# Optimization experiments

Hardware: AMD Instinct MI355X
Metric: run time of the kernel (lower is better)

## Reference

```python
import jax, jax.numpy as jnp
import numpy as np


def gcn_conv(x, edge_index, W, b):
    """PyG GCNConv: linear transform, add self-loops, symmetric D^-1/2 A D^-1/2 aggregation, bias."""
    n = x.shape[0]
    h = x @ W  # [N, out] - transform before propagate (small out dim)
    loop = jnp.arange(n, dtype=edge_index.dtype)
    src = jnp.concatenate([edge_index[0], loop])
    dst = jnp.concatenate([edge_index[1], loop])
    deg = jax.ops.segment_sum(jnp.ones_like(dst, dtype=h.dtype), dst, num_segments=n)
    dinv = jnp.where(deg > 0, jax.lax.rsqrt(deg), 0.0)
    norm = dinv[src] * dinv[dst]  # [E+N]
    out = jax.ops.segment_sum(h[src] * norm[:, None], dst, num_segments=n)
    return out + b


def setup_inputs() -> dict:
    key = jax.random.key(0)
    k1, k2, k3, k4, k5, k6 = jax.random.split(key, 6)
    N, F_in, H, C, E = 100000, 128, 16, 2, 3200000
    x = jax.random.normal(k1, (N, F_in), dtype=jnp.float32)
    edge_index = jax.random.randint(k2, (2, E), 0, N, dtype=jnp.int32)
    # Glorot-style init for GCNConv weights
    W1 = jax.random.normal(k3, (F_in, H), dtype=jnp.float32) * (1.0 / np.sqrt(F_in))
    b1 = jnp.zeros((H,), dtype=jnp.float32)
    W2 = jax.random.normal(k4, (H, C), dtype=jnp.float32) * (1.0 / np.sqrt(H))
    b2 = jnp.zeros((C,), dtype=jnp.float32)
    return {"x": x, "edge_index": edge_index, "W1": W1, "b1": b1, "W2": W2, "b2": b2}


def reference(x, edge_index, W1, b1, W2, b2):
    h = gcn_conv(x, edge_index, W1, b1)
    h = jax.nn.relu(h)
    # F.dropout(training=self.training): eval mode -> identity (deterministic reference)
    h = gcn_conv(h, edge_index, W2, b2)
    return jax.nn.log_softmax(h, axis=1)
```

## Files before the change

kernel.cpp:

```cpp
#include <hip/hip_runtime.h>
#include <hip/hip_bf16.h>
#include <math.h>


#define F_IN 128
#define H1 16
#define C_OUT 2
#define SBS 1024
#define LOG_SBS 10
#define NSB_MAX 128
#define SRC_MASK 0x3FFFFF
#define CH1 4096
#define SLICE 128
#define NSLICE (SBS / SLICE)
#define PCAP 5632

typedef int ix4 __attribute__((ext_vector_type(4)));

__device__ __forceinline__ float bflo(unsigned u) { return __uint_as_float(u << 16); }
__device__ __forceinline__ float bfhi(unsigned u) { return __uint_as_float(u & 0xFFFF0000u); }

__global__ __launch_bounds__(256) void k_cnt(
    const int* __restrict__ dst0, int* __restrict__ cntm, int E, int NSB, int nblk) {
    __shared__ int sc[NSB_MAX];
    int t = threadIdx.x;
    if (t < NSB_MAX) sc[t] = 0;
    __syncthreads();
    int e0 = blockIdx.x * CH1, e1 = min(e0 + CH1, E);
    int n4 = (e1 - e0) >> 2;
    const ix4* d4 = (const ix4*)(dst0 + e0);
    for (int i = t; i < n4; i += 256) {
        ix4 d = __builtin_nontemporal_load(&d4[i]);
        atomicAdd(&sc[((unsigned)d.x) >> LOG_SBS], 1);
        atomicAdd(&sc[((unsigned)d.y) >> LOG_SBS], 1);
        atomicAdd(&sc[((unsigned)d.z) >> LOG_SBS], 1);
        atomicAdd(&sc[((unsigned)d.w) >> LOG_SBS], 1);
    }
    for (int e = e0 + n4 * 4 + t; e < e1; e += 256)
        atomicAdd(&sc[((unsigned)dst0[e]) >> LOG_SBS], 1);
    __syncthreads();
    for (int b = t; b < NSB; b += 256)
        cntm[(size_t)b * nblk + blockIdx.x] = sc[b];
}

__global__ __launch_bounds__(1024) void k_cscan(
    int* __restrict__ cntm, int* __restrict__ tot, int* __restrict__ rp,
    int NSB, int nblk, int E) {
    __shared__ int s[1024];
    int b = blockIdx.x, t = threadIdx.x;
    int* row = cntm + (size_t)b * nblk;
    int own = (t < nblk) ? row[t] : 0;
    s[t] = own;
    __syncthreads();
    for (int off = 1; off < 1024; off <<= 1) {
        int v = (t >= off) ? s[t - off] : 0;
        __syncthreads();
        s[t] += v;
        __syncthreads();
    }
    if (t < nblk) row[t] = s[t] - own;
    if (t == 0) tot[b] = s[1023];
    if (b == 0 && t == 0) rp[NSB * SBS] = E;
}

__global__ __launch_bounds__(256) void k_scat1(
    const int* __restrict__ src0, const int* __restrict__ dst0,
    const int* __restrict__ cntm, unsigned* __restrict__ packed1,
    int E, int NSB, int nblk, int CAP) {
    __shared__ int lcur[NSB_MAX];
    int t = threadIdx.x, blk = blockIdx.x;
    for (int b = t; b < NSB; b += 256)
        lcur[b] = b * CAP + cntm[(size_t)b * nblk + blk];
    __syncthreads();
    int e0 = blk * CH1, e1 = min(e0 + CH1, E);
    int n4 = (e1 - e0) >> 2;
    const ix4* d4 = (const ix4*)(dst0 + e0);
    const ix4* s4 = (const ix4*)(src0 + e0);
    for (int i = t; i < n4; i += 256) {
        ix4 d = __builtin_nontemporal_load(&d4[i]);
        ix4 s = __builtin_nontemporal_load(&s4[i]);
        {
            unsigned dd = (unsigned)d.x;
            int pos = atomicAdd(&lcur[dd >> LOG_SBS], 1);
            packed1[pos] = (unsigned)s.x | ((dd & (SBS - 1)) << 22);
        }
        {
            unsigned dd = (unsigned)d.y;
            int pos = atomicAdd(&lcur[dd >> LOG_SBS], 1);
            packed1[pos] = (unsigned)s.y | ((dd & (SBS - 1)) << 22);
        }
        {
            unsigned dd = (unsigned)d.z;
            int pos = atomicAdd(&lcur[dd >> LOG_SBS], 1);
            packed1[pos] = (unsigned)s.z | ((dd & (SBS - 1)) << 22);
        }
        {
            unsigned dd = (unsigned)d.w;
            int pos = atomicAdd(&lcur[dd >> LOG_SBS], 1);
            packed1[pos] = (unsigned)s.w | ((dd & (SBS - 1)) << 22);
        }
    }
    for (int e = e0 + n4 * 4 + t; e < e1; e += 256) {
        unsigned dd = (unsigned)dst0[e];
        int pos = atomicAdd(&lcur[dd >> LOG_SBS], 1);
        packed1[pos] = (unsigned)src0[e] | ((dd & (SBS - 1)) << 22);
    }
}

__global__ __launch_bounds__(1024) void k_hist(
    const unsigned* __restrict__ packed1, const int* __restrict__ tot,
    int* __restrict__ rp, float* __restrict__ dinv, int N, int NSB, int CAP) {
    __shared__ int cnt[SBS];
    __shared__ int s2[SBS];
    __shared__ int sbase[NSB_MAX];
    int b = blockIdx.x, t = threadIdx.x;
    if (t < NSB_MAX) sbase[t] = (t < NSB) ? tot[t] : 0;
    cnt[t] = 0;
    __syncthreads();
    if (t == 0) {
        int run = 0;
        #pragma unroll 4
        for (int i = 0; i < NSB_MAX; ++i) { int c = sbase[i]; sbase[i] = run; run += c; }
    }
    __syncthreads();
    int cntb = tot[b];
    int e0 = b * CAP, e1 = e0 + cntb;
    int obase = sbase[b];
    int n4 = cntb >> 2;
    const ix4* p4 = (const ix4*)(packed1 + e0);
    for (int i = t; i < n4; i += 1024) {
        ix4 p = p4[i];
        atomicAdd(&cnt[((unsigned)p.x) >> 22], 1);
        atomicAdd(&cnt[((unsigned)p.y) >> 22], 1);
        atomicAdd(&cnt[((unsigned)p.z) >> 22], 1);
        atomicAdd(&cnt[((unsigned)p.w) >> 22], 1);
    }
    for (int e = e0 + n4 * 4 + t; e < e1; e += 1024)
        atomicAdd(&cnt[packed1[e] >> 22], 1);
    __syncthreads();
    int c = cnt[t];
    s2[t] = c;
    __syncthreads();
    for (int off = 1; off < 1024; off <<= 1) {
        int v = (t >= off) ? s2[t - off] : 0;
        __syncthreads();
        s2[t] += v;
        __syncthreads();
    }
    int ep = s2[t] - c;
    int node = (b << LOG_SBS) + t;
    rp[node] = obase + ep;
    if (node < N) dinv[node] = rsqrtf((float)(c + 1));
}

__global__ __launch_bounds__(512) void k_place(
    const unsigned* __restrict__ packed1, const int* __restrict__ tot,
    const int* __restrict__ rp, int* __restrict__ packed2,
    int NSB, int PADB, int CAP) {
    __shared__ int cur[SLICE];
    __shared__ int lbuf[PCAP];
    int bid = blockIdx.x;
    int s = bid / PADB, b = bid - s * PADB;
    if (b >= NSB) return;
    int t = threadIdx.x;
    int node0 = (b << LOG_SBS) + s * SLICE;
    int g0 = rp[node0];
    if (t < SLICE) cur[t] = rp[node0 + t] - g0;
    int slice_len = rp[node0 + SLICE] - g0;
    __syncthreads();
    int cntb = tot[b];
    int e0 = b * CAP, e1 = e0 + cntb;
    int n4 = cntb >> 2;
    const ix4* p4 = (const ix4*)(packed1 + e0);
    for (int i = t; i < n4; i += 512) {
        ix4 p = p4[i];
        {
            unsigned nd = ((unsigned)p.x) >> 22;
            if ((nd >> 7) == (unsigned)s) {
                int pos = atomicAdd(&cur[nd & (SLICE - 1)], 1);
                if (pos < PCAP) lbuf[pos] = p.x & SRC_MASK;
            }
        }
        {
            unsigned nd = ((unsigned)p.y) >> 22;
            if ((nd >> 7) == (unsigned)s) {
                int pos = atomicAdd(&cur[nd & (SLICE - 1)], 1);
                if (pos < PCAP) lbuf[pos] = p.y & SRC_MASK;
            }
        }
        {
            unsigned nd = ((unsigned)p.z) >> 22;
            if ((nd >> 7) == (unsigned)s) {
                int pos = atomicAdd(&cur[nd & (SLICE - 1)], 1);
                if (pos < PCAP) lbuf[pos] = p.z & SRC_MASK;
            }
        }
        {
            unsigned nd = ((unsigned)p.w) >> 22;
            if ((nd >> 7) == (unsigned)s) {
                int pos = atomicAdd(&cur[nd & (SLICE - 1)], 1);
                if (pos < PCAP) lbuf[pos] = p.w & SRC_MASK;
            }
        }
    }
    for (int e = e0 + n4 * 4 + t; e < e1; e += 512) {
        unsigned p = packed1[e];
        unsigned nd = p >> 22;
        if ((nd >> 7) == (unsigned)s) {
            int pos = atomicAdd(&cur[nd & (SLICE - 1)], 1);
            if (pos < PCAP) lbuf[pos] = (int)(p & SRC_MASK);
        }
    }
    __syncthreads();
    int lim = min(slice_len, PCAP);
    for (int i = t; i < lim; i += 512)
        packed2[g0 + i] = lbuf[i];
}

__global__ __launch_bounds__(256) void k_gemm1(
    const float* __restrict__ x, const float* __restrict__ W1,
    const float* __restrict__ dinv, __hip_bfloat16* __restrict__ h1b, int N) {
    __shared__ float w[F_IN * H1];
    __shared__ float xt[16 * F_IN];
    int tid = threadIdx.x;
    int node0 = blockIdx.x * 16;

    const float4* W14 = (const float4*)W1;
    float4* w4 = (float4*)w;
    for (int i = tid; i < F_IN * H1 / 4; i += 256) w4[i] = W14[i];

    const float4* x4 = (const float4*)x;
    float4* xt4 = (float4*)xt;
    for (int i = tid; i < 16 * F_IN / 4; i += 256) {
        int r = i >> 5;
        int node = node0 + r;
        xt4[i] = (node < N) ? x4[(size_t)node * 32 + (i & 31)]
                            : make_float4(0.f, 0.f, 0.f, 0.f);
    }
    __syncthreads();

    int nsub = tid >> 4, f = tid & 15;
    int node = node0 + nsub;
    if (node < N) {
        const float* xr = xt + nsub * F_IN;
        float acc = 0.0f;
        #pragma unroll 16
        for (int k = 0; k < F_IN; ++k)
            acc = fmaf(xr[k], w[k * H1 + f], acc);
        h1b[(size_t)node * H1 + f] = __float2bfloat16(acc * dinv[node]);
    }
}

__global__ __launch_bounds__(256) void k_agg1(
    const int* __restrict__ packed2, const int* __restrict__ rp,
    const __hip_bfloat16* __restrict__ h1b, const float* __restrict__ dinv,
    const float* __restrict__ b1, const float* __restrict__ W2,
    float* __restrict__ h2s, int N) {
    int tid = blockIdx.x * 256 + threadIdx.x;
    int n = tid >> 2, q = tid & 3;
    if (n >= N) return;
    const uint2* hv = (const uint2*)h1b;
    float a[4];
    {
        uint2 s = hv[(size_t)n * 4 + q];
        a[0] = bflo(s.x); a[1] = bfhi(s.x); a[2] = bflo(s.y); a[3] = bfhi(s.y);
    }
    int e = rp[n], e1 = rp[n + 1];
    for (; e + 8 <= e1; e += 8) {
        int p[8];
        #pragma unroll
        for (int u = 0; u < 8; ++u) p[u] = packed2[e + u];
        uint2 v[8];
        #pragma unroll
        for (int u = 0; u < 8; ++u) v[u] = hv[(size_t)p[u] * 4 + q];
        #pragma unroll
        for (int u = 0; u < 8; ++u) {
            a[0] += bflo(v[u].x); a[1] += bfhi(v[u].x);
            a[2] += bflo(v[u].y); a[3] += bfhi(v[u].y);
        }
    }
    for (; e < e1; ++e) {
        uint2 v = hv[(size_t)packed2[e] * 4 + q];
        a[0] += bflo(v.x); a[1] += bfhi(v.x); a[2] += bflo(v.y); a[3] += bfhi(v.y);
    }
    float dv = dinv[n];
    float c0 = 0.f, c1 = 0.f;
    #pragma unroll
    for (int j = 0; j < 4; ++j) {
        int f = q * 4 + j;
        float vv = fmaxf(fmaf(a[j], dv, b1[f]), 0.f);
        c0 = fmaf(vv, W2[f * C_OUT + 0], c0);
        c1 = fmaf(vv, W2[f * C_OUT + 1], c1);
    }
    c0 += __shfl_xor(c0, 1);
    c1 += __shfl_xor(c1, 1);
    c0 += __shfl_xor(c0, 2);
    c1 += __shfl_xor(c1, 2);
    if (q == 0)
        ((float2*)h2s)[n] = make_float2(c0 * dv, c1 * dv);
}

__global__ __launch_bounds__(256) void k_agg2(
    const int* __restrict__ packed2, const int* __restrict__ rp,
    const float* __restrict__ h2s, const float* __restrict__ dinv,
    const float* __restrict__ b2, float* __restrict__ out, int N) {
    int tid = blockIdx.x * 256 + threadIdx.x;
    int n = tid >> 1, q = tid & 1;
    if (n >= N) return;
    float a = h2s[2 * (size_t)n + q];
    int e = rp[n], e1 = rp[n + 1];
    for (; e + 8 <= e1; e += 8) {
        int p[8];
        #pragma unroll
        for (int u = 0; u < 8; ++u) p[u] = packed2[e + u];
        float v[8];
        #pragma unroll
        for (int u = 0; u < 8; ++u) v[u] = h2s[2 * (size_t)p[u] + q];
        #pragma unroll
        for (int u = 0; u < 8; ++u) a += v[u];
    }
    for (; e < e1; ++e) a += h2s[2 * (size_t)packed2[e] + q];
    float dv = dinv[n];
    a = fmaf(a, dv, b2[q]);
    float other = __shfl_xor(a, 1);
    if (q == 0) {
        float a0 = a, a1 = other;
        float m = fmaxf(a0, a1);
        float lse = m + logf(expf(a0 - m) + expf(a1 - m));
        ((float2*)out)[n] = make_float2(a0 - lse, a1 - lse);
    }
}

extern "C" void kernel_launch(void* const* d_in, const int* in_sizes, int n_in,
                              void* d_out, int out_size, void* d_ws, size_t ws_size,
                              hipStream_t stream) {
    const float* x  = (const float*)d_in[0];
    const int* ei   = (const int*)d_in[1];
    const float* W1 = (const float*)d_in[2];
    const float* b1 = (const float*)d_in[3];
    const float* W2 = (const float*)d_in[4];
    const float* b2 = (const float*)d_in[5];
    float* out = (float*)d_out;

    const int N = in_sizes[0] / F_IN;
    const int E = in_sizes[1] / 2;
    const int* src0 = ei;
    const int* dst0 = ei + E;

    const int NSB = (N + SBS - 1) >> LOG_SBS;
    const int nblk = (E + CH1 - 1) / CH1;
    const int PADB = (NSB + 7) & ~7;
    int expSB = (int)(((long long)E << LOG_SBS) / N);
    int CAP = (expSB + expSB / 8 + 2048 + 15) & ~15;

    size_t off = 0;
    float* wsf = (float*)d_ws;
    auto take = [&](size_t nf) { float* p = wsf + off; off += (nf + 3) & ~(size_t)3; return p; };
    float* dinv    = take(N);
    __hip_bfloat16* h1b = (__hip_bfloat16*)take((size_t)N * H1 / 2);
    float* h2s     = take((size_t)N * C_OUT);
    unsigned* packed1 = (unsigned*)take((size_t)NSB * CAP);
    int*   packed2 = (int*)take(E);
    int*   cntm    = (int*)take((size_t)NSB * nblk);
    int*   tot     = (int*)take(NSB_MAX);
    int*   rp      = (int*)take((size_t)NSB * SBS + 1);

    k_cnt<<<nblk, 256, 0, stream>>>(dst0, cntm, E, NSB, nblk);
    k_cscan<<<NSB, 1024, 0, stream>>>(cntm, tot, rp, NSB, nblk, E);
    k_scat1<<<nblk, 256, 0, stream>>>(src0, dst0, cntm, packed1, E, NSB, nblk, CAP);
    k_hist<<<NSB, 1024, 0, stream>>>(packed1, tot, rp, dinv, N, NSB, CAP);
    k_place<<<NSLICE * PADB, 512, 0, stream>>>(packed1, tot, rp, packed2, NSB, PADB, CAP);
    k_gemm1<<<(N + 15) / 16, 256, 0, stream>>>(x, W1, dinv, h1b, N);
    k_agg1<<<(4 * N + 255) / 256, 256, 0, stream>>>(packed2, rp, h1b, dinv, b1, W2, h2s, N);
    k_agg2<<<(2 * N + 255) / 256, 256, 0, stream>>>(packed2, rp, h2s, dinv, b2, out, N);
}
```

Before: 141.0 us.

## Fuse gemm1 into count kernel and aggregation-1 into placement kernel

The dense x@W1 transform now runs as extra blocks of the edge-count kernel, so the two independent stages share one launch. The dinv row scaling of h1 moves into the histogram kernel, which rescales each bf16 row in place once the degree is known. The first aggregation is folded into the placement kernel: each slice gathers neighbours straight from its shared-memory source list instead of re-reading packed2 from global memory. This cuts two launches and one global pass over the edge list. In exchange, the placement kernel gets heavier and relies on slices fitting PCAP, and the extra bf16 rounding step changes numerics slightly.

```diff
diff --git a/kernel.cpp b/kernel.cpp
--- a/kernel.cpp
+++ b/kernel.cpp
@@ -20,27 +20,58 @@
 __device__ __forceinline__ float bflo(unsigned u) { return __uint_as_float(u << 16); }
 __device__ __forceinline__ float bfhi(unsigned u) { return __uint_as_float(u & 0xFFFF0000u); }
 
-__global__ __launch_bounds__(256) void k_cnt(
-    const int* __restrict__ dst0, int* __restrict__ cntm, int E, int NSB, int nblk) {
+__global__ __launch_bounds__(256) void k_cnt_gemm1(
+    const int* __restrict__ dst0, int* __restrict__ cntm,
+    const float* __restrict__ x, const float* __restrict__ W1,
+    __hip_bfloat16* __restrict__ h1b,
+    int E, int NSB, int nblk, int N) {
     __shared__ int sc[NSB_MAX];
+    __shared__ float w[F_IN * H1];
+    __shared__ float xt[16 * F_IN];
     int t = threadIdx.x;
-    if (t < NSB_MAX) sc[t] = 0;
-    __syncthreads();
-    int e0 = blockIdx.x * CH1, e1 = min(e0 + CH1, E);
-    int n4 = (e1 - e0) >> 2;
-    const ix4* d4 = (const ix4*)(dst0 + e0);
-    for (int i = t; i < n4; i += 256) {
-        ix4 d = __builtin_nontemporal_load(&d4[i]);
-        atomicAdd(&sc[((unsigned)d.x) >> LOG_SBS], 1);
-        atomicAdd(&sc[((unsigned)d.y) >> LOG_SBS], 1);
-        atomicAdd(&sc[((unsigned)d.z) >> LOG_SBS], 1);
-        atomicAdd(&sc[((unsigned)d.w) >> LOG_SBS], 1);
-    }
-    for (int e = e0 + n4 * 4 + t; e < e1; e += 256)
-        atomicAdd(&sc[((unsigned)dst0[e]) >> LOG_SBS], 1);
-    __syncthreads();
-    for (int b = t; b < NSB; b += 256)
-        cntm[(size_t)b * nblk + blockIdx.x] = sc[b];
+    if (blockIdx.x < (unsigned)nblk) {
+        if (t < NSB_MAX) sc[t] = 0;
+        __syncthreads();
+        int e0 = blockIdx.x * CH1, e1 = min(e0 + CH1, E);
+        int n4 = (e1 - e0) >> 2;
+        const ix4* d4 = (const ix4*)(dst0 + e0);
+        for (int i = t; i < n4; i += 256) {
+            ix4 d = __builtin_nontemporal_load(&d4[i]);
+            atomicAdd(&sc[((unsigned)d.x) >> LOG_SBS], 1);
+            atomicAdd(&sc[((unsigned)d.y) >> LOG_SBS], 1);
+            atomicAdd(&sc[((unsigned)d.z) >> LOG_SBS], 1);
+            atomicAdd(&sc[((unsigned)d.w) >> LOG_SBS], 1);
+        }
+        for (int e = e0 + n4 * 4 + t; e < e1; e += 256)
+            atomicAdd(&sc[((unsigned)dst0[e]) >> LOG_SBS], 1);
+        __syncthreads();
+        for (int b = t; b < NSB; b += 256)
+            cntm[(size_t)b * nblk + blockIdx.x] = sc[b];
+    } else {
+        int node0 = (blockIdx.x - nblk) * 16;
+        const float4* W14 = (const float4*)W1;
+        float4* w4 = (float4*)w;
+        for (int i = t; i < F_IN * H1 / 4; i += 256) w4[i] = W14[i];
+        const float4* x4 = (const float4*)x;
+        float4* xt4 = (float4*)xt;
+        for (int i = t; i < 16 * F_IN / 4; i += 256) {
+            int r = i >> 5;
+            int node = node0 + r;
+            xt4[i] = (node < N) ? x4[(size_t)node * 32 + (i & 31)]
+                                : make_float4(0.f, 0.f, 0.f, 0.f);
+        }
+        __syncthreads();
+        int nsub = t >> 4, f = t & 15;
+        int node = node0 + nsub;
+        if (node < N) {
+            const float* xr = xt + nsub * F_IN;
+            float acc = 0.0f;
+            #pragma unroll 16
+            for (int k = 0; k < F_IN; ++k)
+                acc = fmaf(xr[k], w[k * H1 + f], acc);
+            h1b[(size_t)node * H1 + f] = __float2bfloat16(acc);
+        }
+    }
 }
 
 __global__ __launch_bounds__(1024) void k_cscan(
@@ -109,7 +140,8 @@
 
 __global__ __launch_bounds__(1024) void k_hist(
     const unsigned* __restrict__ packed1, const int* __restrict__ tot,
-    int* __restrict__ rp, float* __restrict__ dinv, int N, int NSB, int CAP) {
+    int* __restrict__ rp, float* __restrict__ dinv,
+    __hip_bfloat16* __restrict__ h1b, int N, int NSB, int CAP) {
     __shared__ int cnt[SBS];
     __shared__ int s2[SBS];
     __shared__ int sbase[NSB_MAX];
@@ -150,13 +182,32 @@
     int ep = s2[t] - c;
     int node = (b << LOG_SBS) + t;
     rp[node] = obase + ep;
-    if (node < N) dinv[node] = rsqrtf((float)(c + 1));
-}
-
-__global__ __launch_bounds__(512) void k_place(
+    if (node < N) {
+        float dv = rsqrtf((float)(c + 1));
+        dinv[node] = dv;
+        uint4* hrow = (uint4*)(h1b + (size_t)node * H1);
+        uint4 s0 = hrow[0], s1 = hrow[1];
+        unsigned r0[8];
+        float v0, v1;
+        #define SCALE_PACK(word, outi) \
+            v0 = bflo(word) * dv; v1 = bfhi(word) * dv; \
+            r0[outi] = (unsigned)__bfloat16_as_ushort(__float2bfloat16(v0)) | \
+                       ((unsigned)__bfloat16_as_ushort(__float2bfloat16(v1)) << 16);
+        SCALE_PACK(s0.x, 0) SCALE_PACK(s0.y, 1) SCALE_PACK(s0.z, 2) SCALE_PACK(s0.w, 3)
+        SCALE_PACK(s1.x, 4) SCALE_PACK(s1.y, 5) SCALE_PACK(s1.z, 6) SCALE_PACK(s1.w, 7)
+        #undef SCALE_PACK
+        hrow[0] = make_uint4(r0[0], r0[1], r0[2], r0[3]);
+        hrow[1] = make_uint4(r0[4], r0[5], r0[6], r0[7]);
+    }
+}
+
+__global__ __launch_bounds__(512) void k_place_agg1(
     const unsigned* __restrict__ packed1, const int* __restrict__ tot,
     const int* __restrict__ rp, int* __restrict__ packed2,
-    int NSB, int PADB, int CAP) {
+    const __hip_bfloat16* __restrict__ h1b, const float* __restrict__ dinv,
+    const float* __restrict__ b1, const float* __restrict__ W2,
+    float* __restrict__ h2s,
+    int N, int NSB, int PADB, int CAP) {
     __shared__ int cur[SLICE];
     __shared__ int lbuf[PCAP];
     int bid = blockIdx.x;
@@ -215,89 +266,48 @@
     int lim = min(slice_len, PCAP);
     for (int i = t; i < lim; i += 512)
         packed2[g0 + i] = lbuf[i];
-}
-
-__global__ __launch_bounds__(256) void k_gemm1(
-    const float* __restrict__ x, const float* __restrict__ W1,
-    const float* __restrict__ dinv, __hip_bfloat16* __restrict__ h1b, int N) {
-    __shared__ float w[F_IN * H1];
-    __shared__ float xt[16 * F_IN];
-    int tid = threadIdx.x;
-    int node0 = blockIdx.x * 16;
-
-    const float4* W14 = (const float4*)W1;
-    float4* w4 = (float4*)w;
-    for (int i = tid; i < F_IN * H1 / 4; i += 256) w4[i] = W14[i];
-
-    const float4* x4 = (const float4*)x;
-    float4* xt4 = (float4*)xt;
-    for (int i = tid; i < 16 * F_IN / 4; i += 256) {
-        int r = i >> 5;
-        int node = node0 + r;
-        xt4[i] = (node < N) ? x4[(size_t)node * 32 + (i & 31)]
-                            : make_float4(0.f, 0.f, 0.f, 0.f);
-    }
-    __syncthreads();
-
-    int nsub = tid >> 4, f = tid & 15;
-    int node = node0 + nsub;
+    int g = t >> 2, q = t & 3;
+    int node = node0 + g;
     if (node < N) {
-        const float* xr = xt + nsub * F_IN;
-        float acc = 0.0f;
-        #pragma unroll 16
-        for (int k = 0; k < F_IN; ++k)
-            acc = fmaf(xr[k], w[k * H1 + f], acc);
-        h1b[(size_t)node * H1 + f] = __float2bfloat16(acc * dinv[node]);
-    }
-}
-
-__global__ __launch_bounds__(256) void k_agg1(
-    const int* __restrict__ packed2, const int* __restrict__ rp,
-    const __hip_bfloat16* __restrict__ h1b, const float* __restrict__ dinv,
-    const float* __restrict__ b1, const float* __restrict__ W2,
-    float* __restrict__ h2s, int N) {
-    int tid = blockIdx.x * 256 + threadIdx.x;
-    int n = tid >> 2, q = tid & 3;
-    if (n >= N) return;
-    const uint2* hv = (const uint2*)h1b;
-    float a[4];
-    {
-        uint2 s = hv[(size_t)n * 4 + q];
-        a[0] = bflo(s.x); a[1] = bfhi(s.x); a[2] = bflo(s.y); a[3] = bfhi(s.y);
-    }
-    int e = rp[n], e1 = rp[n + 1];
-    for (; e + 8 <= e1; e += 8) {
-        int p[8];
+        const uint2* hv = (const uint2*)h1b;
+        float a[4];
+        uint2 sv = hv[(size_t)node * 4 + q];
+        a[0] = bflo(sv.x); a[1] = bfhi(sv.x); a[2] = bflo(sv.y); a[3] = bfhi(sv.y);
+        int lb = rp[node] - g0;
+        int le = min(rp[node + 1] - g0, PCAP);
+        for (; lb + 8 <= le; lb += 8) {
+            int p[8];
+            #pragma unroll
+            for (int u = 0; u < 8; ++u) p[u] = lbuf[lb + u];
+            uint2 v[8];
+            #pragma unroll
+            for (int u = 0; u < 8; ++u) v[u] = hv[(size_t)p[u] * 4 + q];
+            #pragma unroll
+            for (int u = 0; u < 8; ++u) {
+                a[0] += bflo(v[u].x); a[1] += bfhi(v[u].x);
+                a[2] += bflo(v[u].y); a[3] += bfhi(v[u].y);
+            }
+        }
+        for (; lb < le; ++lb) {
+            uint2 v = hv[(size_t)lbuf[lb] * 4 + q];
+            a[0] += bflo(v.x); a[1] += bfhi(v.x); a[2] += bflo(v.y); a[3] += bfhi(v.y);
+        }
+        float dv = dinv[node];
+        float c0 = 0.f, c1 = 0.f;
         #pragma unroll
-        for (int u = 0; u < 8; ++u) p[u] = packed2[e + u];
-        uint2 v[8];
-        #pragma unroll
-        for (int u = 0; u < 8; ++u) v[u] = hv[(size_t)p[u] * 4 + q];
-        #pragma unroll
-        for (int u = 0; u < 8; ++u) {
-            a[0] += bflo(v[u].x); a[1] += bfhi(v[u].x);
-            a[2] += bflo(v[u].y); a[3] += bfhi(v[u].y);
-        }
-    }
-    for (; e < e1; ++e) {
-        uint2 v = hv[(size_t)packed2[e] * 4 + q];
-        a[0] += bflo(v.x); a[1] += bfhi(v.x); a[2] += bflo(v.y); a[3] += bfhi(v.y);
-    }
-    float dv = dinv[n];
-    float c0 = 0.f, c1 = 0.f;
-    #pragma unroll
-    for (int j = 0; j < 4; ++j) {
-        int f = q * 4 + j;
-        float vv = fmaxf(fmaf(a[j], dv, b1[f]), 0.f);
-        c0 = fmaf(vv, W2[f * C_OUT + 0], c0);
-        c1 = fmaf(vv, W2[f * C_OUT + 1], c1);
-    }
-    c0 += __shfl_xor(c0, 1);
-    c1 += __shfl_xor(c1, 1);
-    c0 += __shfl_xor(c0, 2);
-    c1 += __shfl_xor(c1, 2);
-    if (q == 0)
-        ((float2*)h2s)[n] = make_float2(c0 * dv, c1 * dv);
+        for (int j = 0; j < 4; ++j) {
+            int f = q * 4 + j;
+            float vv = fmaxf(fmaf(a[j], dv, b1[f]), 0.f);
+            c0 = fmaf(vv, W2[f * C_OUT + 0], c0);
+            c1 = fmaf(vv, W2[f * C_OUT + 1], c1);
+        }
+        c0 += __shfl_xor(c0, 1);
+        c1 += __shfl_xor(c1, 1);
+        c0 += __shfl_xor(c0, 2);
+        c1 += __shfl_xor(c1, 2);
+        if (q == 0)
+            ((float2*)h2s)[node] = make_float2(c0 * dv, c1 * dv);
+    }
 }
 
 __global__ __launch_bounds__(256) void k_agg2(
@@ -365,12 +375,12 @@
     int*   tot     = (int*)take(NSB_MAX);
     int*   rp      = (int*)take((size_t)NSB * SBS + 1);
 
-    k_cnt<<<nblk, 256, 0, stream>>>(dst0, cntm, E, NSB, nblk);
+    int nbGemm = (N + 15) / 16;
+    k_cnt_gemm1<<<nblk + nbGemm, 256, 0, stream>>>(dst0, cntm, x, W1, h1b, E, NSB, nblk, N);
     k_cscan<<<NSB, 1024, 0, stream>>>(cntm, tot, rp, NSB, nblk, E);
     k_scat1<<<nblk, 256, 0, stream>>>(src0, dst0, cntm, packed1, E, NSB, nblk, CAP);
-    k_hist<<<NSB, 1024, 0, stream>>>(packed1, tot, rp, dinv, N, NSB, CAP);
-    k_place<<<NSLICE * PADB, 512, 0, stream>>>(packed1, tot, rp, packed2, NSB, PADB, CAP);
-    k_gemm1<<<(N + 15) / 16, 256, 0, stream>>>(x, W1, dinv, h1b, N);
-    k_agg1<<<(4 * N + 255) / 256, 256, 0, stream>>>(packed2, rp, h1b, dinv, b1, W2, h2s, N);
+    k_hist<<<NSB, 1024, 0, stream>>>(packed1, tot, rp, dinv, h1b, N, NSB, CAP);
+    k_place_agg1<<<NSLICE * PADB, 512, 0, stream>>>(packed1, tot, rp, packed2,
+                                                    h1b, dinv, b1, W2, h2s, N, NSB, PADB, CAP);
     k_agg2<<<(2 * N + 255) / 256, 256, 0, stream>>>(packed2, rp, h2s, dinv, b2, out, N);
 }
```

After: 128.1 us. 1.1x faster.
